# Kernel tuning notes

Measured on AMD Instinct MI355X. Metric: run time of the kernel, lower is better.

The kernel has to match this reference:

```python
import jax, jax.numpy as jnp
import numpy as np

N, E, D, NINP, V, T, L, B = 60000, 200000, 128, 256, 15000, 6, 2, 16


def setup_inputs() -> dict:
    key = jax.random.key(0)
    k = jax.random.split(key, 16)
    s = 0.05
    return {
        "word_ids": jax.random.randint(k[0], (N,), 0, V),
        "src": jax.random.randint(k[1], (E,), 0, N),
        "dst": jax.random.randint(k[2], (E,), 0, N),
        "edge_time": jax.random.randint(k[3], (E,), 0, T),
        "edge_weight": jax.random.uniform(k[4], (E,), jnp.float32),
        "graph_id": jnp.sort(jax.random.randint(k[5], (N,), 0, B)),
        "y_data": jax.random.uniform(k[6], (B,), jnp.float32),
        "word_embeds": jax.random.normal(k[7], (V, NINP), jnp.float32) * s,
        "adapt_W": jax.random.normal(k[8], (NINP, D), jnp.float32) * s,
        "adapt_b": jnp.zeros((D,), jnp.float32),
        "gcn_weights": jax.random.normal(k[9], (L, D, D), jnp.float32) * s,
        "lstm_Wih": jax.random.normal(k[10], (L, 4 * D, D), jnp.float32) * s,
        "lstm_Whh": jax.random.normal(k[11], (L, 4 * D, D), jnp.float32) * s,
        "lstm_bih": jnp.zeros((L, 4 * D), jnp.float32),
        "lstm_bhh": jnp.zeros((L, 4 * D), jnp.float32),
        "out_W": jax.random.normal(k[12], (D, 1), jnp.float32) * s,
        "out_b": jnp.zeros((1,), jnp.float32),
    }


def _lstm_cell(x, h, c, Wih, Whh, bih, bhh):
    # torch.nn.LSTMCell math; gate order i, f, g, o
    g = x @ Wih.T + bih + h @ Whh.T + bhh
    i, f, gg, o = jnp.split(g, 4, axis=-1)
    c2 = jax.nn.sigmoid(f) * c + jax.nn.sigmoid(i) * jnp.tanh(gg)
    return jax.nn.sigmoid(o) * jnp.tanh(c2), c2


def _forward(word_ids, src, dst, edge_time, edge_weight, graph_id, y_data,
             word_embeds, adapt_W, adapt_b, gcn_weights,
             lstm_Wih, lstm_Whh, lstm_bih, lstm_bhh, out_W, out_b):
    h0 = word_embeds[word_ids] @ adapt_W + adapt_b  # adapt_ws, (N, D)
    z = jnp.zeros((D, D), h0.dtype)  # LSTM zero state (batch of D rows)

    def step(carry, t):
        h, hx, cx0, first = carry
        em = edge_time == t                       # edges in time-t subgraph
        has = em.any()
        ef = jnp.where(em, edge_weight, jnp.zeros((), edge_weight.dtype))
        mark = em.astype(h.dtype)
        deg = jnp.zeros((N,), h.dtype).at[src].add(mark).at[dst].add(mark)
        touched = (deg > 0) & has                 # endpoints of time-t edges
        ht = h
        hx_new, cx_new = [], []
        for i in range(L):
            h_zero, c_zero = _lstm_cell(hx[i], z, z, lstm_Wih[i], lstm_Whh[i], lstm_bih[i], lstm_bhh[i])
            h_st, _ = _lstm_cell(hx[i], hx[i], cx0[i], lstm_Wih[i], lstm_Whh[i], lstm_bih[i], lstm_bhh[i])
            hi = jnp.where(first, h_st, h_zero)
            ci = jnp.where(first, cx0[i], c_zero)  # faithful: cx frozen at the first active step (original indexing bug)
            hi = jnp.where(has, hi, hx[i])         # layer skipped if no edges at t
            ci = jnp.where(has, ci, cx0[i])
            hx_new.append(hi)
            cx_new.append(ci)
            hw = ht @ hi                           # mm(h, evolved weight)
            msg = hw[src] * ef[:, None]            # u_mul_e('h','weight')
            agg = jnp.zeros_like(ht).at[dst].add(msg)  # sum aggregation
            ht = jnp.maximum(agg, 0.0)             # relu activation (dropout=0)
        h = jnp.where(touched[:, None], ht, h)     # write back subgraph nodes
        first = first | has
        return (h, jnp.stack(hx_new), jnp.stack(cx_new), first), None

    init = (h0, gcn_weights, jnp.zeros_like(gcn_weights), jnp.asarray(False))
    (h, _, _, _), _ = jax.lax.scan(step, init, jnp.arange(T))

    pooled = jax.ops.segment_max(h, graph_id, num_segments=B)  # dgl.max_nodes
    pooled = jnp.where(jnp.isfinite(pooled), pooled, 0.0)  # guard (segments are non-empty in practice)
    logits = (pooled @ out_W + out_b).reshape(-1)
    # binary_cross_entropy_with_logits, mean reduction
    loss = jnp.mean(jnp.maximum(logits, 0.0) - logits * y_data + jnp.log1p(jnp.exp(-jnp.abs(logits))))
    return loss, jax.nn.sigmoid(logits)


def reference(word_ids, src, dst, edge_time, edge_weight, graph_id, y_data,
              word_embeds, adapt_W, adapt_b, gcn_weights,
              lstm_Wih, lstm_Whh, lstm_bih, lstm_bhh, out_W, out_b):
    return _forward(word_ids, src, dst, edge_time, edge_weight, graph_id, y_data,
                    word_embeds, adapt_W, adapt_b, gcn_weights,
                    lstm_Wih, lstm_Whh, lstm_bih, lstm_bhh, out_W, out_b)
```

## Files before the change

### kernel.cpp

```cpp
#include <hip/hip_runtime.h>
#include <hip/hip_bf16.h>
#include <math.h>

#define N_NODES 60000
#define E_EDGES 200000
#define DIM     128
#define NINPK   256
#define TSTEPS  6
#define LLAYERS 2
#define BGRAPH  16
#define NBINS   (TSTEPS * N_NODES)
#define NB      ((NBINS + 1023) / 1024)
#define NWORDS  15000

#define B_INITP  ((NBINS + 255) / 256)
#define B_PREP   16
#define B_HIST   ((E_EDGES + 255) / 256)
#define B_TGEMM  ((NWORDS + 127) / 128)
#define B_PLACE2 ((E_EDGES + 1023) / 1024)
#define B_EMBED  512
#define B_LSTM5  64
#define GB       ((N_NODES + 127) / 128)
#define B_ZZ     64
#define B_SEGMAX ((N_NODES + 127) / 128)

typedef float f32x4 __attribute__((ext_vector_type(4)));
typedef short s16x8 __attribute__((ext_vector_type(8)));
typedef short s16x4 __attribute__((ext_vector_type(4)));

static __device__ __forceinline__ float sigm(float x) { return 1.f / (1.f + expf(-x)); }

static __device__ __forceinline__ short f2bf(float f) {
  unsigned u = __float_as_uint(f);
  u += 0x7FFFu + ((u >> 16) & 1u);
  return (short)(u >> 16);
}
static __device__ __forceinline__ float bf2f(short s) {
  return __uint_as_float(((unsigned)(unsigned short)s) << 16);
}
static __device__ __forceinline__ unsigned fenc(float f) {
  unsigned u = __float_as_uint(f);
  return (u & 0x80000000u) ? ~u : (u | 0x80000000u);
}
static __device__ __forceinline__ float fdec(unsigned u) {
  u = (u & 0x80000000u) ? (u & 0x7fffffffu) : ~u;
  return __uint_as_float(u);
}


template <bool RELU, bool BIAS, bool GOUT>
static __device__ __forceinline__ void gemm_compute_epi256(
    f32x4 (&acc)[2][8], const short* WtKt, const float* bias, short* C16,
    const int* dstmap, int N, int n0, const short* As, int rsg, int ktg,
    short* Ws, bool last) {
  const int tid = threadIdx.x;
  const int lane = tid & 63;
  const int w = tid >> 6;
  __syncthreads();
  const int4* wg = reinterpret_cast<const int4*>(WtKt);
  int4* wl = reinterpret_cast<int4*>(Ws);
#pragma unroll
  for (int p = 0; p < 4; ++p) wl[p * 256 + tid] = wg[p * 256 + tid];
  __syncthreads();
#pragma unroll
  for (int kk = 0; kk < 2; ++kk) {
    int gb = kk * 4 + (lane >> 4);
    s16x8 a[2];
#pragma unroll
    for (int fr = 0; fr < 2; ++fr) {
      int row = w * 32 + fr * 16 + (lane & 15);
      a[fr] = *(const s16x8*)&As[(row * rsg + ktg + (gb ^ (row & 7))) * 8];
    }
#pragma unroll
    for (int fc = 0; fc < 8; ++fc) {
      int col = fc * 16 + (lane & 15);
      s16x8 b = *(const s16x8*)&Ws[(col * 8 + (gb ^ (col & 7))) * 8];
      acc[0][fc] = __builtin_amdgcn_mfma_f32_16x16x32_bf16(a[0], b, acc[0][fc], 0, 0, 0);
      acc[1][fc] = __builtin_amdgcn_mfma_f32_16x16x32_bf16(a[1], b, acc[1][fc], 0, 0, 0);
    }
  }
  if (!last) return;
  const int cb = lane & 15;
  const int rb = w * 32 + (lane >> 4) * 4;
#pragma unroll
  for (int fr = 0; fr < 2; ++fr) {
#pragma unroll
    for (int reg = 0; reg < 4; ++reg) {
      int n = n0 + rb + fr * 16 + reg;
      if (n >= N) continue;
      long drow = GOUT ? (long)dstmap[n] : (long)n;
      short* cp = C16 + drow * DIM;
#pragma unroll
      for (int fc = 0; fc < 8; ++fc) {
        float x = acc[fr][fc][reg];
        if (BIAS) x += bias[fc * 16 + cb];
        if (RELU) x = fmaxf(x, 0.f);
        cp[fc * 16 + cb] = f2bf(x);
      }
    }
  }
}

template <bool PACKEDIN, bool GOUT>
static __device__ __forceinline__ void fusedgemm512(
    const int* __restrict__ ss, const int* __restrict__ sl,
    const int2* __restrict__ sedge, const short* __restrict__ IN16,
    const int* __restrict__ ro, const short* __restrict__ Wt,
    short* __restrict__ C16, const int* __restrict__ sd,
    const int* __restrict__ nsegp, short* As2, short* Ws, int bid) {
  const int N = nsegp[0];
  const int n0 = bid * 128;
  if (n0 >= N) return;
  const int tid = threadIdx.x;
  const int lane16 = tid & 15;
  const int grp = tid >> 4;
  int st[4], ln[4];
#pragma unroll
  for (int it = 0; it < 4; ++it) {
    int seg = n0 + it * 32 + grp;
    bool ok = seg < N;
    st[it] = ok ? ss[seg] : 0;
    ln[it] = ok ? sl[seg] : 0;
  }
  int2 e0[4];
#pragma unroll
  for (int it = 0; it < 4; ++it)
    e0[it] = ln[it] ? sedge[st[it]] : make_int2(0, 0);
  int r0[4];
#pragma unroll
  for (int it = 0; it < 4; ++it)
    r0[it] = ln[it] ? (PACKEDIN ? ro[e0[it].x] : e0[it].x) : -1;
  s16x8 h0[4];
#pragma unroll
  for (int it = 0; it < 4; ++it) {
    s16x8 z = {};
    h0[it] = (r0[it] >= 0) ? *(const s16x8*)&IN16[(long)r0[it] * DIM + lane16 * 8] : z;
  }
#pragma unroll
  for (int it = 0; it < 4; ++it) {
    int row = it * 32 + grp;
    float a0 = 0, a1 = 0, a2 = 0, a3 = 0, a4 = 0, a5 = 0, a6 = 0, a7 = 0;
    if (ln[it] && r0[it] >= 0) {
      float w = __int_as_float(e0[it].y);
      a0 = w * bf2f(h0[it][0]); a1 = w * bf2f(h0[it][1]);
      a2 = w * bf2f(h0[it][2]); a3 = w * bf2f(h0[it][3]);
      a4 = w * bf2f(h0[it][4]); a5 = w * bf2f(h0[it][5]);
      a6 = w * bf2f(h0[it][6]); a7 = w * bf2f(h0[it][7]);
    }
    for (int e = st[it] + 1; e < st[it] + ln[it]; ++e) {
      int2 v = sedge[e];
      int r2 = PACKEDIN ? ro[v.x] : v.x;
      if (PACKEDIN && r2 < 0) continue;
      float w = __int_as_float(v.y);
      s16x8 hv = *(const s16x8*)&IN16[(long)r2 * DIM + lane16 * 8];
      a0 = fmaf(w, bf2f(hv[0]), a0); a1 = fmaf(w, bf2f(hv[1]), a1);
      a2 = fmaf(w, bf2f(hv[2]), a2); a3 = fmaf(w, bf2f(hv[3]), a3);
      a4 = fmaf(w, bf2f(hv[4]), a4); a5 = fmaf(w, bf2f(hv[5]), a5);
      a6 = fmaf(w, bf2f(hv[6]), a6); a7 = fmaf(w, bf2f(hv[7]), a7);
    }
    s16x8 outv;
    outv[0] = f2bf(a0); outv[1] = f2bf(a1); outv[2] = f2bf(a2); outv[3] = f2bf(a3);
    outv[4] = f2bf(a4); outv[5] = f2bf(a5); outv[6] = f2bf(a6); outv[7] = f2bf(a7);
    int slot = (lane16 & 8) | ((lane16 & 7) ^ (row & 7));
    *(s16x8*)&As2[(row * 16 + slot) * 8] = outv;
  }
  const int lane = tid & 63;
  const int w = tid >> 6;
  f32x4 acc[8] = {};
#pragma unroll
  for (int kt = 0; kt < 2; ++kt) {
    __syncthreads();
    const int4* wg = reinterpret_cast<const int4*>(Wt + kt * 128 * 64);
    int4* wl = reinterpret_cast<int4*>(Ws);
#pragma unroll
    for (int p = 0; p < 2; ++p) wl[p * 512 + tid] = wg[p * 512 + tid];
    __syncthreads();
#pragma unroll
    for (int kk = 0; kk < 2; ++kk) {
      int gb = kk * 4 + (lane >> 4);
      int row = w * 16 + (lane & 15);
      s16x8 a = *(const s16x8*)&As2[(row * 16 + kt * 8 + (gb ^ (row & 7))) * 8];
#pragma unroll
      for (int fc = 0; fc < 8; ++fc) {
        int col = fc * 16 + (lane & 15);
        s16x8 b = *(const s16x8*)&Ws[(col * 8 + (gb ^ (col & 7))) * 8];
        acc[fc] = __builtin_amdgcn_mfma_f32_16x16x32_bf16(a, b, acc[fc], 0, 0, 0);
      }
    }
  }
  const int cb = lane & 15;
  const int rb = w * 16 + (lane >> 4) * 4;
#pragma unroll
  for (int reg = 0; reg < 4; ++reg) {
    int n = n0 + rb + reg;
    if (n >= N) continue;
    long drow = GOUT ? (long)sd[n] : (long)n;
    short* cp = C16 + drow * DIM;
#pragma unroll
    for (int fc = 0; fc < 8; ++fc) {
      float x = fmaxf(acc[fc][reg], 0.f);
      cp[fc * 16 + cb] = f2bf(x);
    }
  }
}

static __device__ __forceinline__ void tablegemm_body(
    const float* __restrict__ Af, const short* __restrict__ Wt,
    const float* __restrict__ bias, short* __restrict__ table16, short* As,
    short* Ws, int bid) {
  const int n0 = bid * 128;
  const int tid = threadIdx.x;
  f32x4 acc[2][8] = {};
#pragma unroll
  for (int kt = 0; kt < 4; ++kt) {
    __syncthreads();
#pragma unroll
    for (int p = 0; p < 4; ++p) {
      int gi = p * 256 + tid;
      int row = gi >> 3, s = gi & 7;
      int n = n0 + row;
      s16x8 v = {};
      if (n < NWORDS) {
        const float* ap = Af + (long)n * NINPK + kt * 64 + (s ^ (row & 7)) * 8;
        float4 v0 = *reinterpret_cast<const float4*>(ap);
        float4 v1 = *reinterpret_cast<const float4*>(ap + 4);
        v[0] = f2bf(v0.x); v[1] = f2bf(v0.y); v[2] = f2bf(v0.z); v[3] = f2bf(v0.w);
        v[4] = f2bf(v1.x); v[5] = f2bf(v1.y); v[6] = f2bf(v1.z); v[7] = f2bf(v1.w);
      }
      *(s16x8*)&As[(row * 8 + s) * 8] = v;
    }
    gemm_compute_epi256<false, true, false>(acc, Wt + kt * 128 * 64, bias, table16,
                                            nullptr, NWORDS, n0, As, 8, 0, Ws,
                                            kt == 3);
  }
}

static __device__ __forceinline__ void zzero_body(short* __restrict__ hb,
                                                  const int* __restrict__ zl,
                                                  const int* __restrict__ nzp,
                                                  int bid, int nblocks) {
  int nz = nzp[0];
  int l = threadIdx.x & 15;
  s16x8 z = {};
  for (int s = bid * 32 + (threadIdx.x >> 4); s < nz; s += nblocks * 32) {
    *reinterpret_cast<s16x8*>(&hb[(long)zl[s] * DIM + l * 8]) = z;
  }
}

static __device__ __forceinline__ void lstm_body512(
    int bid, const float* __restrict__ hxc, float* __restrict__ hxn,
    float* __restrict__ cx, const float* __restrict__ Wih,
    const float* __restrict__ Whh, const float* __restrict__ bih,
    const float* __restrict__ bhh, const int* __restrict__ meta,
    short* __restrict__ WtBase, int k, float* wi, float* wh) {
  int tid = threadIdx.x;
  int i = bid >> 5;
  int j4 = bid & 31;
  int jl = tid >> 7;
  int r = tid & 127;
  int j = j4 * 4 + jl;
  float* wiL = wi + jl * 512;
  float* whL = wh + jl * 512;
#pragma unroll
  for (int g4 = 0; g4 < 4; ++g4) {
    wiL[g4 * 128 + r] = Wih[((long)i * 512 + g4 * 128 + j) * DIM + r];
    whL[g4 * 128 + r] = Whh[((long)i * 512 + g4 * 128 + j) * DIM + r];
  }
  __syncthreads();
  const float4* x4 = reinterpret_cast<const float4*>(hxc + ((long)i * DIM + r) * DIM);
  float a0 = 0, a1 = 0, a2 = 0, a3 = 0, b0 = 0, b1 = 0, b2 = 0, b3 = 0;
#pragma unroll 4
  for (int k4 = 0; k4 < 32; ++k4) {
    float4 xv = x4[k4];
    const float* vp = &xv.x;
#pragma unroll
    for (int q = 0; q < 4; ++q) {
      int kk = k4 * 4 + q;
      float xs = vp[q];
      a0 = fmaf(xs, wiL[kk], a0);       a1 = fmaf(xs, wiL[128 + kk], a1);
      a2 = fmaf(xs, wiL[256 + kk], a2); a3 = fmaf(xs, wiL[384 + kk], a3);
      b0 = fmaf(xs, whL[kk], b0);       b1 = fmaf(xs, whL[128 + kk], b1);
      b2 = fmaf(xs, whL[256 + kk], b2); b3 = fmaf(xs, whL[384 + kk], b3);
    }
  }
  int cbi = i * 512 + j;
  float g0i = a0 + bih[cbi] + bhh[cbi];
  float g0f = a1 + bih[cbi + 128] + bhh[cbi + 128];
  float g0g = a2 + bih[cbi + 256] + bhh[cbi + 256];
  float g0o = a3 + bih[cbi + 384] + bhh[cbi + 384];
  float g1i = g0i + b0, g1f = g0f + b1, g1g = g0g + b2, g1o = g0o + b3;
  int idx = i * 16384 + r * 128 + j;
  float c0v = cx[idx];
  float c_zero = sigm(g0i) * tanhf(g0g);
  float h_zero = sigm(g0o) * tanhf(c_zero);
  float c_st = sigm(g1f) * c0v + sigm(g1i) * tanhf(g1g);
  float h_st = sigm(g1o) * tanhf(c_st);
  int first = meta[8 + k];
  int has = meta[k] > 0;
  float hi_v = first ? h_st : h_zero;
  float ci_v = first ? c0v : c_zero;
  float xj = reinterpret_cast<const float*>(x4)[j];
  float hnew = has ? hi_v : xj;
  float cnew = has ? ci_v : c0v;
  hxn[idx] = hnew;
  cx[idx] = cnew;
  short* Wt = WtBase + i * 16384;
  int kb = r >> 6, g = (r >> 3) & 7, jj = r & 7;
  Wt[((kb * DIM + j) * 8 + (g ^ (j & 7))) * 8 + jj] = f2bf(hnew);
}


__global__ void k_setup0(const float* __restrict__ gcn, float* __restrict__ hxA,
                         float* __restrict__ cx, int* __restrict__ meta,
                         unsigned* __restrict__ keys, int* __restrict__ hist,
                         unsigned* __restrict__ flagbits,
                         const float* __restrict__ adW, short* __restrict__ WtAd) {
  int bid = blockIdx.x;
  int tid = threadIdx.x;
  if (bid < B_INITP) {
    int i = bid * 256 + tid;
    if (i < LLAYERS * DIM * DIM) { hxA[i] = gcn[i]; cx[i] = 0.f; }
    if (i < BGRAPH * DIM) keys[i] = 0u;
    if (i < 64) meta[i] = 0;
    if (i < NBINS) hist[i] = 0;
    if (i < (NBINS + 31) / 32) flagbits[i] = 0u;
  } else {
    int idx = (bid - B_INITP) * 256 + tid;
    int g = idx & 7;
    int c = (idx >> 3) & 127;
    int kb = idx >> 10;
    s16x8 s;
#pragma unroll
    for (int j = 0; j < 8; ++j) s[j] = f2bf(adW[(long)(kb * 64 + g * 8 + j) * DIM + c]);
    *(s16x8*)&WtAd[(((long)kb * DIM + c) * 8 + (g ^ (c & 7))) * 8] = s;
  }
}

__global__ __launch_bounds__(256) void k_histg(
    const int* __restrict__ et, const int* __restrict__ src,
    const int* __restrict__ dst, int* __restrict__ hist,
    unsigned* __restrict__ flagbits, const float* __restrict__ wemb,
    const short* __restrict__ WtAd, const float* __restrict__ adb,
    short* __restrict__ table16) {
  __shared__ short As[128 * 64];
  __shared__ short Ws[128 * 64];
  int bid = blockIdx.x;
  if (bid < B_HIST) {
    int e = bid * 256 + threadIdx.x;
    if (e < E_EDGES) {
      int t = et[e];
      atomicAdd(&hist[t * N_NODES + dst[e]], 1);
      int fs = t * N_NODES + src[e];
      atomicOr(&flagbits[fs >> 5], 1u << (fs & 31));
    }
  } else {
    tablegemm_body(wemb, WtAd, adb, table16, As, Ws, bid - B_HIST);
  }
}

__global__ void k_scan1b(const int* __restrict__ hist,
                         const unsigned* __restrict__ flagbits,
                         int* __restrict__ scanA, int* __restrict__ scanB,
                         int* __restrict__ scanC, int* __restrict__ bsumA,
                         int* __restrict__ bsumB, int* __restrict__ bsumC) {
  __shared__ int shA[256], shB[256], shC[256];
  int b0 = blockIdx.x * 1024;
  int tid = threadIdx.x;
  int v[4], w[4], z[4];
  int sA = 0, sB = 0, sC = 0;
#pragma unroll
  for (int q = 0; q < 4; ++q) {
    int i = b0 + tid * 4 + q;
    int c = (i < NBINS) ? hist[i] : 0;
    int fl = (i < NBINS) ? (int)((flagbits[i >> 5] >> (i & 31)) & 1u) : 0;
    v[q] = c; w[q] = (c > 0) ? 1 : 0; z[q] = (fl && c == 0) ? 1 : 0;
    sA += c; sB += w[q]; sC += z[q];
  }
  shA[tid] = sA; shB[tid] = sB; shC[tid] = sC;
  __syncthreads();
  for (int off = 1; off < 256; off <<= 1) {
    int xA = (tid >= off) ? shA[tid - off] : 0;
    int xB = (tid >= off) ? shB[tid - off] : 0;
    int xC = (tid >= off) ? shC[tid - off] : 0;
    __syncthreads();
    shA[tid] += xA; shB[tid] += xB; shC[tid] += xC;
    __syncthreads();
  }
  int exA = shA[tid] - sA, exB = shB[tid] - sB, exC = shC[tid] - sC;
#pragma unroll
  for (int q = 0; q < 4; ++q) {
    int i = b0 + tid * 4 + q;
    if (i < NBINS) { scanA[i] = exA; scanB[i] = exB; scanC[i] = exC; }
    exA += v[q]; exB += w[q]; exC += z[q];
  }
  if (tid == 255) {
    bsumA[blockIdx.x] = shA[255];
    bsumB[blockIdx.x] = shB[255];
    bsumC[blockIdx.x] = shC[255];
  }
}

__global__ __launch_bounds__(256) void k_scan2p(
    int* __restrict__ bsumA, int* __restrict__ bsumB, int* __restrict__ bsumC,
    const int* __restrict__ scanA, const int* __restrict__ scanB,
    const int* __restrict__ scanC, int* __restrict__ meta) {
  __shared__ int pA[256], pB[256], pC[256];
  __shared__ int eA[512], eB[512], eC[512];
  int tid = threadIdx.x;
  int i0 = tid * 2, i1 = tid * 2 + 1;
  int a0 = (i0 < NB) ? bsumA[i0] : 0, a1 = (i1 < NB) ? bsumA[i1] : 0;
  int b0 = (i0 < NB) ? bsumB[i0] : 0, b1 = (i1 < NB) ? bsumB[i1] : 0;
  int c0 = (i0 < NB) ? bsumC[i0] : 0, c1 = (i1 < NB) ? bsumC[i1] : 0;
  int tA = a0 + a1, tB = b0 + b1, tC = c0 + c1;
  pA[tid] = tA; pB[tid] = tB; pC[tid] = tC;
  __syncthreads();
  for (int off = 1; off < 256; off <<= 1) {
    int xA = (tid >= off) ? pA[tid - off] : 0;
    int xB = (tid >= off) ? pB[tid - off] : 0;
    int xC = (tid >= off) ? pC[tid - off] : 0;
    __syncthreads();
    pA[tid] += xA; pB[tid] += xB; pC[tid] += xC;
    __syncthreads();
  }
  int baseA = pA[tid] - tA, baseB = pB[tid] - tB, baseC = pC[tid] - tC;
  eA[i0] = baseA; eA[i1] = baseA + a0;
  eB[i0] = baseB; eB[i1] = baseB + b0;
  eC[i0] = baseC; eC[i1] = baseC + c0;
  if (i0 < NB) { bsumA[i0] = baseA; bsumB[i0] = baseB; bsumC[i0] = baseC; }
  if (i1 < NB) { bsumA[i1] = baseA + a0; bsumB[i1] = baseB + b0; bsumC[i1] = baseC + c0; }
  __syncthreads();
  if (tid == 0) {
    int loA[TSTEPS + 1], loB[TSTEPS + 1], loC[TSTEPS + 1];
    for (int t = 0; t < TSTEPS; ++t) {
      int ib = t * N_NODES, blk = ib >> 10;
      loA[t] = scanA[ib] + eA[blk];
      loB[t] = scanB[ib] + eB[blk];
      loC[t] = scanC[ib] + eC[blk];
    }
    loA[TSTEPS] = pA[255]; loB[TSTEPS] = pB[255]; loC[TSTEPS] = pC[255];
    int f = 0;
    for (int t = 0; t < TSTEPS; ++t) {
      int cnt = loA[t + 1] - loA[t];
      meta[t] = cnt;
      meta[8 + t] = f; f |= (cnt > 0);
      meta[32 + t] = loB[t + 1] - loB[t];
      meta[48 + t] = loB[t];
      meta[40 + t] = loC[t + 1] - loC[t];
      meta[56 + t] = loC[t];
    }
  }
}

__global__ void k_scan3seg(int* __restrict__ scanA, const int* __restrict__ bsumA,
                           const int* __restrict__ scanB, const int* __restrict__ bsumB,
                           const int* __restrict__ scanC, const int* __restrict__ bsumC,
                           const int* __restrict__ hist,
                           const unsigned* __restrict__ flagbits,
                           const int* __restrict__ meta, int* __restrict__ segdst,
                           int* __restrict__ segstart, int* __restrict__ seglen,
                           int* __restrict__ rowof, int* __restrict__ zlist) {
  int i = blockIdx.x * blockDim.x + threadIdx.x;
  if (i >= NBINS) return;
  int vA = scanA[i] + bsumA[i >> 10];
  scanA[i] = vA;
  int c = hist[i];
  int t = i / N_NODES;
  int tb = t * N_NODES;
  if (c > 0) {
    int sidx = scanB[i] + bsumB[i >> 10] - meta[48 + t];
    long sb = (long)tb + sidx;
    segdst[sb] = i - tb;
    segstart[sb] = vA;
    seglen[sb] = c;
    rowof[i] = sidx;
  } else {
    rowof[i] = -1;
    if ((flagbits[i >> 5] >> (i & 31)) & 1u) {
      int zr = scanC[i] + bsumC[i >> 10] - meta[56 + t];
      zlist[(long)tb + zr] = i - tb;
    }
  }
}

__global__ __launch_bounds__(512) void k_setup1(
    const int* __restrict__ et, const int* __restrict__ src,
    const int* __restrict__ dst, const float* __restrict__ ew,
    int* __restrict__ scanA, int2* __restrict__ sedge,
    const short* __restrict__ table16, const int* __restrict__ wid,
    short* __restrict__ hb, const float* __restrict__ hxA, float* __restrict__ hxB,
    float* __restrict__ cx, const float* __restrict__ Wih,
    const float* __restrict__ Whh, const float* __restrict__ bih,
    const float* __restrict__ bhh, const int* __restrict__ meta,
    short* __restrict__ WtT) {
  __shared__ float lb[4096];
  int bid = blockIdx.x;
  int tid = threadIdx.x;
  if (bid < B_PLACE2) {
    int e0 = bid * 1024 + tid;
    int e1 = e0 + 512;
    bool ok0 = e0 < E_EDGES, ok1 = e1 < E_EDGES;
    int t0 = ok0 ? et[e0] : 0, t1 = ok1 ? et[e1] : 0;
    int d0 = ok0 ? dst[e0] : 0, d1 = ok1 ? dst[e1] : 0;
    int s0 = ok0 ? src[e0] : 0, s1 = ok1 ? src[e1] : 0;
    float w0 = ok0 ? ew[e0] : 0.f, w1 = ok1 ? ew[e1] : 0.f;
    int p0 = ok0 ? atomicAdd(&scanA[t0 * N_NODES + d0], 1) : 0;
    int p1 = ok1 ? atomicAdd(&scanA[t1 * N_NODES + d1], 1) : 0;
    if (ok0) sedge[p0] = make_int2(s0, __float_as_int(w0));
    if (ok1) sedge[p1] = make_int2(s1, __float_as_int(w1));
  } else if (bid < B_PLACE2 + B_EMBED) {
    int l = tid & 15;
    for (int n = (bid - B_PLACE2) * 32 + (tid >> 4); n < N_NODES; n += B_EMBED * 32) {
      *reinterpret_cast<s16x8*>(&hb[(long)n * DIM + l * 8]) =
          *reinterpret_cast<const s16x8*>(&table16[(long)wid[n] * DIM + l * 8]);
    }
  } else {
    lstm_body512(bid - B_PLACE2 - B_EMBED, hxA, hxB, cx, Wih, Whh, bih, bhh, meta,
                 WtT, 0, lb, lb + 2048);
  }
}

__global__ __launch_bounds__(512) void k_A(
    const int* __restrict__ ss, const int* __restrict__ sl,
    const int2* __restrict__ sedge, const short* __restrict__ hb,
    const short* __restrict__ Wt0, short* __restrict__ P2b,
    const int* __restrict__ nsegp, const float* __restrict__ hxc,
    float* __restrict__ hxn, float* __restrict__ cx,
    const float* __restrict__ Wih, const float* __restrict__ Whh,
    const float* __restrict__ bih, const float* __restrict__ bhh,
    const int* __restrict__ meta, short* __restrict__ WtNext, int k) {
  __shared__ short As2[128 * 128];
  __shared__ short Ws[128 * 64];
  int bid = blockIdx.x;
  if (bid < GB) {
    fusedgemm512<false, false>(ss, sl, sedge, hb, nullptr, Wt0, P2b, nullptr,
                               nsegp, As2, Ws, bid);
  } else if (k < TSTEPS) {
    float* lb = (float*)As2;
    lstm_body512(bid - GB, hxc, hxn, cx, Wih, Whh, bih, bhh, meta, WtNext, k,
                 lb, lb + 2048);
  }
}

__global__ __launch_bounds__(512) void k_B(
    const int* __restrict__ ss, const int* __restrict__ sl,
    const int2* __restrict__ sedge, const short* __restrict__ P2b,
    const int* __restrict__ ro, const short* __restrict__ Wt1,
    short* __restrict__ hb, const int* __restrict__ sd,
    const int* __restrict__ nsegp, const int* __restrict__ zl,
    const int* __restrict__ nzp) {
  __shared__ short As2[128 * 128];
  __shared__ short Ws[128 * 64];
  int bid = blockIdx.x;
  if (bid < GB) {
    fusedgemm512<true, true>(ss, sl, sedge, P2b, ro, Wt1, hb, sd, nsegp,
                             As2, Ws, bid);
  } else {
    zzero_body(hb, zl, nzp, bid - GB, B_ZZ);
  }
}

__global__ __launch_bounds__(256) void k_segmax(
    const short* __restrict__ hb, const int* __restrict__ gid,
    unsigned* __restrict__ keys) {
  __shared__ float red[256 * 8];
  int tid = threadIdx.x;
  int c = tid & 15;
  int r = tid >> 4;
  int n0 = blockIdx.x * 128;
  int nend = min(n0 + 128, N_NODES);
  float m[8];
#pragma unroll
  for (int j = 0; j < 8; ++j) m[j] = -INFINITY;
  if (gid[n0] == gid[nend - 1]) {
    int g = gid[n0];
#pragma unroll
    for (int it = 0; it < 8; ++it) {
      int n = n0 + it * 16 + r;
      if (n < N_NODES) {
        s16x8 v = *(const s16x8*)&hb[(long)n * DIM + c * 8];
#pragma unroll
        for (int j = 0; j < 8; ++j) m[j] = fmaxf(m[j], bf2f(v[j]));
      }
    }
#pragma unroll
    for (int j = 0; j < 8; ++j) red[tid * 8 + j] = m[j];
    __syncthreads();
    for (int off = 8; off >= 1; off >>= 1) {
      if (r < off) {
#pragma unroll
        for (int j = 0; j < 8; ++j)
          red[tid * 8 + j] = fmaxf(red[tid * 8 + j], red[(tid + off * 16) * 8 + j]);
      }
      __syncthreads();
    }
    if (r == 0) {
#pragma unroll
      for (int j = 0; j < 8; ++j)
        atomicMax(&keys[(long)g * DIM + c * 8 + j], fenc(red[tid * 8 + j]));
    }
  } else {
    int curg = -1;
#pragma unroll
    for (int it = 0; it < 8; ++it) {
      int n = n0 + it * 16 + r;
      if (n >= N_NODES) break;
      int g = gid[n];
      if (g != curg) {
        if (curg >= 0) {
#pragma unroll
          for (int j = 0; j < 8; ++j)
            atomicMax(&keys[(long)curg * DIM + c * 8 + j], fenc(m[j]));
        }
        curg = g;
#pragma unroll
        for (int j = 0; j < 8; ++j) m[j] = -INFINITY;
      }
      s16x8 v = *(const s16x8*)&hb[(long)n * DIM + c * 8];
#pragma unroll
      for (int j = 0; j < 8; ++j) m[j] = fmaxf(m[j], bf2f(v[j]));
    }
    if (curg >= 0) {
#pragma unroll
      for (int j = 0; j < 8; ++j)
        atomicMax(&keys[(long)curg * DIM + c * 8 + j], fenc(m[j]));
    }
  }
}

__global__ void k_final(const unsigned* __restrict__ keys, const float* __restrict__ outW,
                        const float* __restrict__ outB, const float* __restrict__ y,
                        float* __restrict__ out) {
  __shared__ float lt[BGRAPH];
  int tid = threadIdx.x;
  int b = tid >> 2, l4 = tid & 3;
  float s = 0.f;
  for (int d = l4; d < DIM; d += 4) {
    float v = fdec(keys[(long)b * DIM + d]);
    if (!isfinite(v)) v = 0.f;
    s += v * outW[d];
  }
  s += __shfl_down(s, 1);
  s += __shfl_down(s, 2);
  if (l4 == 0) {
    float l = s + outB[0];
    out[1 + b] = 1.f / (1.f + expf(-l));
    lt[b] = fmaxf(l, 0.f) - l * y[b] + log1pf(expf(-fabsf(l)));
  }
  __syncthreads();
  if (tid == 0) {
    float acc = 0.f;
    for (int i = 0; i < BGRAPH; ++i) acc += lt[i];
    out[0] = acc / (float)BGRAPH;
  }
}

extern "C" void kernel_launch(void* const* d_in, const int* in_sizes, int n_in,
                              void* d_out, int out_size, void* d_ws, size_t ws_size,
                              hipStream_t stream) {
  const int* word_ids = (const int*)d_in[0];
  const int* src = (const int*)d_in[1];
  const int* dst = (const int*)d_in[2];
  const int* et = (const int*)d_in[3];
  const float* ew = (const float*)d_in[4];
  const int* gid = (const int*)d_in[5];
  const float* y = (const float*)d_in[6];
  const float* wemb = (const float*)d_in[7];
  const float* adW = (const float*)d_in[8];
  const float* adb = (const float*)d_in[9];
  const float* gcn = (const float*)d_in[10];
  const float* Wih = (const float*)d_in[11];
  const float* Whh = (const float*)d_in[12];
  const float* bih = (const float*)d_in[13];
  const float* bhh = (const float*)d_in[14];
  const float* outW = (const float*)d_in[15];
  const float* outB = (const float*)d_in[16];
  float* out = (float*)d_out;

  char* ws = (char*)d_ws;
  const long ND = (long)N_NODES * DIM;
  short* hb = (short*)ws;       ws += ND * 2;
  short* P2b = (short*)ws;      ws += ND * 2;
  float* hxA = (float*)ws;      ws += LLAYERS * DIM * DIM * 4;
  float* hxB = (float*)ws;      ws += LLAYERS * DIM * DIM * 4;
  float* cx = (float*)ws;       ws += LLAYERS * DIM * DIM * 4;
  int* meta = (int*)ws;         ws += 64 * 4;
  unsigned* keys = (unsigned*)ws; ws += BGRAPH * DIM * 4;
  int* hist = (int*)ws;         ws += (long)NBINS * 4;
  int* scanA = (int*)ws;        ws += (long)NBINS * 4;
  int* scanB = (int*)ws;        ws += (long)NBINS * 4;
  int* scanC = (int*)ws;        ws += (long)NBINS * 4;
  int* bsumA = (int*)ws;        ws += ((NB + 63) & ~63) * 4;
  int* bsumB = (int*)ws;        ws += ((NB + 63) & ~63) * 4;
  int* bsumC = (int*)ws;        ws += ((NB + 63) & ~63) * 4;
  int* rowof = (int*)ws;        ws += (long)NBINS * 4;
  int* segdst = (int*)ws;       ws += (long)NBINS * 4;
  int* segstart = (int*)ws;     ws += (long)NBINS * 4;
  int* seglen = (int*)ws;       ws += (long)NBINS * 4;
  int* zlist = (int*)ws;        ws += (long)NBINS * 4;
  int2* sedge = (int2*)ws;      ws += (long)E_EDGES * 8;
  unsigned* flagbits = (unsigned*)ws; ws += ((NBINS + 31) / 32 + 64) * 4;
  short* table16 = (short*)ws;  ws += (long)NWORDS * DIM * 2;
  short* WtAd = (short*)ws;     ws += 4L * DIM * 64 * 2;
  short* WtT = (short*)ws;      ws += 7L * 2 * 16384 * 2;

  k_setup0<<<B_INITP + B_PREP, 256, 0, stream>>>(gcn, hxA, cx, meta, keys, hist,
                                                 flagbits, adW, WtAd);
  k_histg<<<B_HIST + B_TGEMM, 256, 0, stream>>>(et, src, dst, hist, flagbits,
                                                wemb, WtAd, adb, table16);
  k_scan1b<<<NB, 256, 0, stream>>>(hist, flagbits, scanA, scanB, scanC,
                                   bsumA, bsumB, bsumC);
  k_scan2p<<<1, 256, 0, stream>>>(bsumA, bsumB, bsumC, scanA, scanB, scanC, meta);
  k_scan3seg<<<B_INITP, 256, 0, stream>>>(scanA, bsumA, scanB, bsumB, scanC, bsumC,
                                          hist, flagbits, meta, segdst, segstart,
                                          seglen, rowof, zlist);
  k_setup1<<<B_PLACE2 + B_EMBED + B_LSTM5, 512, 0, stream>>>(
      et, src, dst, ew, scanA, sedge, table16, word_ids, hb, hxA, hxB, cx,
      Wih, Whh, bih, bhh, meta, WtT);

  for (int t = 0; t < TSTEPS; ++t) {
    const int* nsegp = &meta[32 + t];
    const int* nzp = &meta[40 + t];
    const int* ss = segstart + (long)t * N_NODES;
    const int* sl = seglen + (long)t * N_NODES;
    const int* sd = segdst + (long)t * N_NODES;
    const int* ro = rowof + (long)t * N_NODES;
    const int* zl = zlist + (long)t * N_NODES;
    int k = t + 1;
    const float* hxc = (k & 1) ? hxB : hxA;
    float* hxn = (k & 1) ? hxA : hxB;
    k_A<<<GB + B_LSTM5, 512, 0, stream>>>(
        ss, sl, sedge, hb, WtT + (long)t * 2 * 16384, P2b, nsegp,
        hxc, hxn, cx, Wih, Whh, bih, bhh, meta, WtT + (long)k * 2 * 16384, k);
    k_B<<<GB + B_ZZ, 512, 0, stream>>>(
        ss, sl, sedge, P2b, ro, WtT + ((long)t * 2 + 1) * 16384, hb, sd, nsegp,
        zl, nzp);
  }

  k_segmax<<<B_SEGMAX, 256, 0, stream>>>(hb, gid, keys);
  k_final<<<1, 64, 0, stream>>>(keys, outW, outB, y, out);
}
```

Before: 303.7 us.

## Prefetch GEMM weights into registers and fold block-sum scan into segment kernel

```diff
diff --git a/kernel.cpp b/kernel.cpp
--- a/kernel.cpp
+++ b/kernel.cpp
@@ -114,6 +114,13 @@
   const int tid = threadIdx.x;
   const int lane16 = tid & 15;
   const int grp = tid >> 4;
+  int4 wr00, wr01, wr10, wr11;
+  {
+    const int4* wg0 = reinterpret_cast<const int4*>(Wt);
+    const int4* wg1 = reinterpret_cast<const int4*>(Wt + 128 * 64);
+    wr00 = wg0[tid]; wr01 = wg0[512 + tid];
+    wr10 = wg1[tid]; wr11 = wg1[512 + tid];
+  }
   int st[4], ln[4];
 #pragma unroll
   for (int it = 0; it < 4; ++it) {
@@ -164,16 +171,13 @@
     int slot = (lane16 & 8) | ((lane16 & 7) ^ (row & 7));
     *(s16x8*)&As2[(row * 16 + slot) * 8] = outv;
   }
+  int4* wl = reinterpret_cast<int4*>(Ws);
+  wl[tid] = wr00; wl[512 + tid] = wr01;
   const int lane = tid & 63;
   const int w = tid >> 6;
   f32x4 acc[8] = {};
 #pragma unroll
   for (int kt = 0; kt < 2; ++kt) {
-    __syncthreads();
-    const int4* wg = reinterpret_cast<const int4*>(Wt + kt * 128 * 64);
-    int4* wl = reinterpret_cast<int4*>(Ws);
-#pragma unroll
-    for (int p = 0; p < 2; ++p) wl[p * 512 + tid] = wg[p * 512 + tid];
     __syncthreads();
 #pragma unroll
     for (int kk = 0; kk < 2; ++kk) {
@@ -186,6 +190,10 @@
         s16x8 b = *(const s16x8*)&Ws[(col * 8 + (gb ^ (col & 7))) * 8];
         acc[fc] = __builtin_amdgcn_mfma_f32_16x16x32_bf16(a, b, acc[fc], 0, 0, 0);
       }
+    }
+    if (kt == 0) {
+      __syncthreads();
+      wl[tid] = wr10; wl[512 + tid] = wr11;
     }
   }
   const int cb = lane & 15;
@@ -400,84 +408,78 @@
   }
 }
 
-__global__ __launch_bounds__(256) void k_scan2p(
-    int* __restrict__ bsumA, int* __restrict__ bsumB, int* __restrict__ bsumC,
-    const int* __restrict__ scanA, const int* __restrict__ scanB,
-    const int* __restrict__ scanC, int* __restrict__ meta) {
-  __shared__ int pA[256], pB[256], pC[256];
-  __shared__ int eA[512], eB[512], eC[512];
+__global__ __launch_bounds__(256) void k_scan3seg(
+    const int* __restrict__ scanA, const int* __restrict__ bsumA,
+    const int* __restrict__ scanB, const int* __restrict__ bsumB,
+    const int* __restrict__ scanC, const int* __restrict__ bsumC,
+    const int* __restrict__ hist, const unsigned* __restrict__ flagbits,
+    int* __restrict__ scanD, int* __restrict__ segdst, int* __restrict__ segstart,
+    int* __restrict__ seglen, int* __restrict__ rowof, int* __restrict__ zlist,
+    int* __restrict__ meta) {
+  __shared__ int sA[512], sB[512], sC[512];
   int tid = threadIdx.x;
-  int i0 = tid * 2, i1 = tid * 2 + 1;
-  int a0 = (i0 < NB) ? bsumA[i0] : 0, a1 = (i1 < NB) ? bsumA[i1] : 0;
-  int b0 = (i0 < NB) ? bsumB[i0] : 0, b1 = (i1 < NB) ? bsumB[i1] : 0;
-  int c0 = (i0 < NB) ? bsumC[i0] : 0, c1 = (i1 < NB) ? bsumC[i1] : 0;
-  int tA = a0 + a1, tB = b0 + b1, tC = c0 + c1;
-  pA[tid] = tA; pB[tid] = tB; pC[tid] = tC;
+  for (int q = tid; q < 512; q += 256) {
+    sA[q] = (q < NB) ? bsumA[q] : 0;
+    sB[q] = (q < NB) ? bsumB[q] : 0;
+    sC[q] = (q < NB) ? bsumC[q] : 0;
+  }
   __syncthreads();
-  for (int off = 1; off < 256; off <<= 1) {
-    int xA = (tid >= off) ? pA[tid - off] : 0;
-    int xB = (tid >= off) ? pB[tid - off] : 0;
-    int xC = (tid >= off) ? pC[tid - off] : 0;
+  for (int off = 1; off < 512; off <<= 1) {
+    int q0 = tid, q1 = tid + 256;
+    int a0 = (q0 >= off) ? sA[q0 - off] : 0, b0 = (q0 >= off) ? sB[q0 - off] : 0,
+        c0 = (q0 >= off) ? sC[q0 - off] : 0;
+    int a1 = (q1 >= off) ? sA[q1 - off] : 0, b1 = (q1 >= off) ? sB[q1 - off] : 0,
+        c1 = (q1 >= off) ? sC[q1 - off] : 0;
     __syncthreads();
-    pA[tid] += xA; pB[tid] += xB; pC[tid] += xC;
+    sA[q0] += a0; sB[q0] += b0; sC[q0] += c0;
+    sA[q1] += a1; sB[q1] += b1; sC[q1] += c1;
     __syncthreads();
   }
-  int baseA = pA[tid] - tA, baseB = pB[tid] - tB, baseC = pC[tid] - tC;
-  eA[i0] = baseA; eA[i1] = baseA + a0;
-  eB[i0] = baseB; eB[i1] = baseB + b0;
-  eC[i0] = baseC; eC[i1] = baseC + c0;
-  if (i0 < NB) { bsumA[i0] = baseA; bsumB[i0] = baseB; bsumC[i0] = baseC; }
-  if (i1 < NB) { bsumA[i1] = baseA + a0; bsumB[i1] = baseB + b0; bsumC[i1] = baseC + c0; }
-  __syncthreads();
-  if (tid == 0) {
+  int i = blockIdx.x * 256 + tid;
+  if (i < NBINS) {
+    int blk = i >> 10;
+    int eAx = blk ? sA[blk - 1] : 0;
+    int eBx = blk ? sB[blk - 1] : 0;
+    int eCx = blk ? sC[blk - 1] : 0;
+    int t = i / N_NODES;
+    int tb = t * N_NODES;
+    int blkT = tb >> 10;
+    int vA = scanA[i] + eAx;
+    scanD[i] = vA;
+    int c = hist[i];
+    if (c > 0) {
+      int baseB = scanB[tb] + (blkT ? sB[blkT - 1] : 0);
+      int sidx = scanB[i] + eBx - baseB;
+      long sb = (long)tb + sidx;
+      segdst[sb] = i - tb;
+      segstart[sb] = vA;
+      seglen[sb] = c;
+      rowof[i] = sidx;
+    } else {
+      rowof[i] = -1;
+      if ((flagbits[i >> 5] >> (i & 31)) & 1u) {
+        int baseC = scanC[tb] + (blkT ? sC[blkT - 1] : 0);
+        int zr = scanC[i] + eCx - baseC;
+        zlist[(long)tb + zr] = i - tb;
+      }
+    }
+  }
+  if (blockIdx.x == 0 && tid == 0) {
     int loA[TSTEPS + 1], loB[TSTEPS + 1], loC[TSTEPS + 1];
     for (int t = 0; t < TSTEPS; ++t) {
       int ib = t * N_NODES, blk = ib >> 10;
-      loA[t] = scanA[ib] + eA[blk];
-      loB[t] = scanB[ib] + eB[blk];
-      loC[t] = scanC[ib] + eC[blk];
-    }
-    loA[TSTEPS] = pA[255]; loB[TSTEPS] = pB[255]; loC[TSTEPS] = pC[255];
+      loA[t] = scanA[ib] + (blk ? sA[blk - 1] : 0);
+      loB[t] = scanB[ib] + (blk ? sB[blk - 1] : 0);
+      loC[t] = scanC[ib] + (blk ? sC[blk - 1] : 0);
+    }
+    loA[TSTEPS] = sA[NB - 1]; loB[TSTEPS] = sB[NB - 1]; loC[TSTEPS] = sC[NB - 1];
     int f = 0;
     for (int t = 0; t < TSTEPS; ++t) {
       int cnt = loA[t + 1] - loA[t];
       meta[t] = cnt;
       meta[8 + t] = f; f |= (cnt > 0);
       meta[32 + t] = loB[t + 1] - loB[t];
-      meta[48 + t] = loB[t];
       meta[40 + t] = loC[t + 1] - loC[t];
-      meta[56 + t] = loC[t];
-    }
-  }
-}
-
-__global__ void k_scan3seg(int* __restrict__ scanA, const int* __restrict__ bsumA,
-                           const int* __restrict__ scanB, const int* __restrict__ bsumB,
-                           const int* __restrict__ scanC, const int* __restrict__ bsumC,
-                           const int* __restrict__ hist,
-                           const unsigned* __restrict__ flagbits,
-                           const int* __restrict__ meta, int* __restrict__ segdst,
-                           int* __restrict__ segstart, int* __restrict__ seglen,
-                           int* __restrict__ rowof, int* __restrict__ zlist) {
-  int i = blockIdx.x * blockDim.x + threadIdx.x;
-  if (i >= NBINS) return;
-  int vA = scanA[i] + bsumA[i >> 10];
-  scanA[i] = vA;
-  int c = hist[i];
-  int t = i / N_NODES;
-  int tb = t * N_NODES;
-  if (c > 0) {
-    int sidx = scanB[i] + bsumB[i >> 10] - meta[48 + t];
-    long sb = (long)tb + sidx;
-    segdst[sb] = i - tb;
-    segstart[sb] = vA;
-    seglen[sb] = c;
-    rowof[i] = sidx;
-  } else {
-    rowof[i] = -1;
-    if ((flagbits[i >> 5] >> (i & 31)) & 1u) {
-      int zr = scanC[i] + bsumC[i >> 10] - meta[56 + t];
-      zlist[(long)tb + zr] = i - tb;
     }
   }
 }
@@ -485,7 +487,7 @@
 __global__ __launch_bounds__(512) void k_setup1(
     const int* __restrict__ et, const int* __restrict__ src,
     const int* __restrict__ dst, const float* __restrict__ ew,
-    int* __restrict__ scanA, int2* __restrict__ sedge,
+    int* __restrict__ scanD, int2* __restrict__ sedge,
     const short* __restrict__ table16, const int* __restrict__ wid,
     short* __restrict__ hb, const float* __restrict__ hxA, float* __restrict__ hxB,
     float* __restrict__ cx, const float* __restrict__ Wih,
@@ -503,8 +505,8 @@
     int d0 = ok0 ? dst[e0] : 0, d1 = ok1 ? dst[e1] : 0;
     int s0 = ok0 ? src[e0] : 0, s1 = ok1 ? src[e1] : 0;
     float w0 = ok0 ? ew[e0] : 0.f, w1 = ok1 ? ew[e1] : 0.f;
-    int p0 = ok0 ? atomicAdd(&scanA[t0 * N_NODES + d0], 1) : 0;
-    int p1 = ok1 ? atomicAdd(&scanA[t1 * N_NODES + d1], 1) : 0;
+    int p0 = ok0 ? atomicAdd(&scanD[t0 * N_NODES + d0], 1) : 0;
+    int p1 = ok1 ? atomicAdd(&scanD[t1 * N_NODES + d1], 1) : 0;
     if (ok0) sedge[p0] = make_int2(s0, __float_as_int(w0));
     if (ok1) sedge[p1] = make_int2(s1, __float_as_int(w1));
   } else if (bid < B_PLACE2 + B_EMBED) {
@@ -689,6 +691,7 @@
   int* scanA = (int*)ws;        ws += (long)NBINS * 4;
   int* scanB = (int*)ws;        ws += (long)NBINS * 4;
   int* scanC = (int*)ws;        ws += (long)NBINS * 4;
+  int* scanD = (int*)ws;        ws += (long)NBINS * 4;
   int* bsumA = (int*)ws;        ws += ((NB + 63) & ~63) * 4;
   int* bsumB = (int*)ws;        ws += ((NB + 63) & ~63) * 4;
   int* bsumC = (int*)ws;        ws += ((NB + 63) & ~63) * 4;
@@ -709,12 +712,11 @@
                                                 wemb, WtAd, adb, table16);
   k_scan1b<<<NB, 256, 0, stream>>>(hist, flagbits, scanA, scanB, scanC,
                                    bsumA, bsumB, bsumC);
-  k_scan2p<<<1, 256, 0, stream>>>(bsumA, bsumB, bsumC, scanA, scanB, scanC, meta);
   k_scan3seg<<<B_INITP, 256, 0, stream>>>(scanA, bsumA, scanB, bsumB, scanC, bsumC,
-                                          hist, flagbits, meta, segdst, segstart,
-                                          seglen, rowof, zlist);
+                                          hist, flagbits, scanD, segdst, segstart,
+                                          seglen, rowof, zlist, meta);
   k_setup1<<<B_PLACE2 + B_EMBED + B_LSTM5, 512, 0, stream>>>(
-      et, src, dst, ew, scanA, sedge, table16, word_ids, hb, hxA, hxB, cx,
+      et, src, dst, ew, scanD, sedge, table16, word_ids, hb, hxA, hxB, cx,
       Wih, Whh, bih, bhh, meta, WtT);
 
   for (int t = 0; t < TSTEPS; ++t) {
```

Result: no change. 305.2 us (+0.5%).
